# Performance work log

Measured on AMD Instinct MI355X. Metric: run time of the kernel, lower is better.

The kernel has to match this reference:

```python
import jax, jax.numpy as jnp
import numpy as np

IRREPS = [0, 1, 2, 3, 4]   # l values; dim = sum(2l+1) = 25
MAX_L = max(IRREPS)
DIM = sum(2 * l + 1 for l in IRREPS)
EPS = 1e-14
N_POINTS = 200000


def _p_terms(i, a, b, l):
    """Ivanic-Ruedenberg P(i,l,a,b) as sparse terms: (coef, flat idx into R1 (3x3), flat idx into D^{l-1})."""
    lp = l - 1
    n = 2 * lp + 1
    row = i + 1  # R1 rows/cols indexed by m in {-1,0,1} -> {0,1,2}
    if b == l:
        return [(1.0, row * 3 + 2, (a + lp) * n + 2 * lp),
                (-1.0, row * 3 + 0, (a + lp) * n + 0)]
    if b == -l:
        return [(1.0, row * 3 + 2, (a + lp) * n + 0),
                (1.0, row * 3 + 0, (a + lp) * n + 2 * lp)]
    return [(1.0, row * 3 + 1, (a + lp) * n + (b + lp))]


def _ru_tables(l):
    """Precompute sparse recurrence tables for building D^l from D^{l-1} and R1."""
    out_idx, rij, ab, coef = [], [], [], []
    n = 2 * l + 1
    for m in range(-l, l + 1):
        for mp in range(-l, l + 1):
            denom = (2 * l) * (2 * l - 1) if abs(mp) == l else (l + mp) * (l - mp)
            d0 = 1.0 if m == 0 else 0.0
            u = np.sqrt((l + m) * (l - m) / denom)
            v = 0.5 * np.sqrt((1 + d0) * (l + abs(m) - 1) * (l + abs(m)) / denom) * (1 - 2 * d0)
            w = -0.5 * np.sqrt(max(l - abs(m) - 1, 0) * (l - abs(m)) / denom) * (1 - d0)
            terms = []
            if u != 0.0:
                terms += [(u * c, i, j) for c, i, j in _p_terms(0, m, mp, l)]
            if v != 0.0:
                if m == 0:
                    terms += [(v * c, i, j) for c, i, j in _p_terms(1, 1, mp, l)]
                    terms += [(v * c, i, j) for c, i, j in _p_terms(-1, -1, mp, l)]
                elif m > 0:
                    s = np.sqrt(2.0) if m == 1 else 1.0
                    terms += [(v * s * c, i, j) for c, i, j in _p_terms(1, m - 1, mp, l)]
                    if m != 1:
                        terms += [(-v * c, i, j) for c, i, j in _p_terms(-1, -m + 1, mp, l)]
                else:
                    if m != -1:
                        terms += [(v * c, i, j) for c, i, j in _p_terms(1, m + 1, mp, l)]
                    s = np.sqrt(2.0) if m == -1 else 1.0
                    terms += [(v * s * c, i, j) for c, i, j in _p_terms(-1, -m - 1, mp, l)]
            if w != 0.0:
                if m > 0:
                    terms += [(w * c, i, j) for c, i, j in _p_terms(1, m + 1, mp, l)]
                    terms += [(w * c, i, j) for c, i, j in _p_terms(-1, -m - 1, mp, l)]
                else:
                    terms += [(w * c, i, j) for c, i, j in _p_terms(1, m - 1, mp, l)]
                    terms += [(-w * c, i, j) for c, i, j in _p_terms(-1, -m + 1, mp, l)]
            o = (m + l) * n + (mp + l)
            for c, i, j in terms:
                out_idx.append(o); rij.append(i); ab.append(j); coef.append(c)
    return (np.asarray(out_idx), np.asarray(rij), np.asarray(ab),
            np.asarray(coef, dtype=np.float32))


_TABLES = {l: _ru_tables(l) for l in range(2, MAX_L + 1)}


def _wigner_blocks(R1, max_l):
    """D^l for real spherical harmonics via Ivanic-Ruedenberg recurrence. R1: (N,3,3)."""
    N = R1.shape[0]
    blocks = {0: jnp.ones((N, 1, 1), R1.dtype), 1: R1}
    r1f = R1.reshape(N, 9)
    for l in range(2, max_l + 1):
        oi, rij, ab, cf = _TABLES[l]
        dprev = blocks[l - 1].reshape(N, (2 * l - 1) ** 2)
        contrib = cf[None, :] * r1f[:, rij] * dprev[:, ab]  # (N, n_terms)
        n = 2 * l + 1
        Dl = jnp.zeros((N, n * n), R1.dtype).at[:, oi].add(contrib)
        blocks[l] = Dl.reshape(N, n, n)
    return blocks


def _forward(xyz):
    # angles of v (normalized=True): theta polar, phi azimuthal
    norm = jnp.linalg.norm(xyz, axis=-1, keepdims=True)
    v = xyz / jnp.maximum(norm, EPS)
    ct = jnp.clip(v[..., 2], -1.0, 1.0)
    theta = jnp.arccos(ct)
    phi = jnp.arctan2(v[..., 1], v[..., 0])
    st, cp, sp = jnp.sin(theta), jnp.cos(phi), jnp.sin(phi)
    z = jnp.zeros_like(ct)
    # R = Ry(-theta) @ Rz(-phi): R @ v = |v| z_hat
    R = jnp.stack([
        jnp.stack([ct * cp, ct * sp, -st], -1),
        jnp.stack([-sp, cp, z], -1),
        jnp.stack([st * cp, st * sp, ct], -1),
    ], -2)  # (N,3,3)
    # real-SH l=1 basis order m=(-1,0,1) <-> (y,z,x)
    p = jnp.array([1, 2, 0])
    R1 = R[:, p][:, :, p]
    blocks = _wigner_blocks(R1, MAX_L)
    N = xyz.shape[0]
    D = jnp.zeros((N, DIM, DIM), xyz.dtype)
    off = 0
    for l in IRREPS:
        d = 2 * l + 1
        D = D.at[:, off:off + d, off:off + d].set(blocks[l])
        off += d
    return D


def setup_inputs() -> dict:
    key = jax.random.key(0)
    xyz = jax.random.normal(key, (N_POINTS, 3), dtype=jnp.float32)
    return {"xyz": xyz}


def reference(xyz):
    return _forward(xyz)
```

## Files before the change

kernel.cpp:

```cpp
#include <hip/hip_runtime.h>
#include <utility>
#include <cstddef>


struct Term { int o; int r; int a; float c; };
struct LTable { int n; Term t[1024]; };

constexpr double csqrt(double x) {
    if (x <= 0.0) return 0.0;
    double g = x < 1.0 ? 1.0 : x;
    for (int i = 0; i < 50; ++i) g = 0.5 * (g + x / g);
    return g;
}
constexpr int cabs_i(int x) { return x < 0 ? -x : x; }
constexpr int cmax_i(int a, int b) { return a > b ? a : b; }

constexpr void add_p(LTable& T, int o, double scale, int i, int a, int b, int l) {
    int lp = l - 1;
    int np = 2 * lp + 1;
    int row = i + 1;
    if (b == l) {
        T.t[T.n++] = Term{o, row * 3 + 2, (a + lp) * np + 2 * lp, (float)scale};
        T.t[T.n++] = Term{o, row * 3 + 0, (a + lp) * np + 0,      (float)(-scale)};
    } else if (b == -l) {
        T.t[T.n++] = Term{o, row * 3 + 2, (a + lp) * np + 0,      (float)scale};
        T.t[T.n++] = Term{o, row * 3 + 0, (a + lp) * np + 2 * lp, (float)scale};
    } else {
        T.t[T.n++] = Term{o, row * 3 + 1, (a + lp) * np + (b + lp), (float)scale};
    }
}

constexpr LTable ru_table(int l) {
    LTable T{};
    int n = 2 * l + 1;
    for (int m = -l; m <= l; ++m) {
        for (int mp = -l; mp <= l; ++mp) {
            double denom = (cabs_i(mp) == l) ? (double)((2 * l) * (2 * l - 1))
                                             : (double)((l + mp) * (l - mp));
            double d0 = (m == 0) ? 1.0 : 0.0;
            double u = csqrt((double)((l + m) * (l - m)) / denom);
            double v = 0.5 * csqrt((1.0 + d0) * (l + cabs_i(m) - 1) * (l + cabs_i(m)) / denom)
                       * (1.0 - 2.0 * d0);
            double w = -0.5 * csqrt((double)cmax_i(l - cabs_i(m) - 1, 0) * (l - cabs_i(m)) / denom)
                       * (1.0 - d0);
            int o = (m + l) * n + (mp + l);
            if (u != 0.0) add_p(T, o, u, 0, m, mp, l);
            if (v != 0.0) {
                if (m == 0) {
                    add_p(T, o, v, 1, 1, mp, l);
                    add_p(T, o, v, -1, -1, mp, l);
                } else if (m > 0) {
                    double s = (m == 1) ? csqrt(2.0) : 1.0;
                    add_p(T, o, v * s, 1, m - 1, mp, l);
                    if (m != 1) add_p(T, o, -v, -1, -m + 1, mp, l);
                } else {
                    if (m != -1) add_p(T, o, v, 1, m + 1, mp, l);
                    double s = (m == -1) ? csqrt(2.0) : 1.0;
                    add_p(T, o, v * s, -1, -m - 1, mp, l);
                }
            }
            if (w != 0.0) {
                if (m > 0) {
                    add_p(T, o, w, 1, m + 1, mp, l);
                    add_p(T, o, w, -1, -m - 1, mp, l);
                } else {
                    add_p(T, o, w, 1, m - 1, mp, l);
                    add_p(T, o, -w, -1, -m + 1, mp, l);
                }
            }
        }
    }
    return T;
}

inline constexpr LTable T2 = ru_table(2);
inline constexpr LTable T3 = ru_table(3);
inline constexpr LTable T4 = ru_table(4);

template<const LTable& T>
constexpr int er_start(int e) {
    for (int i = 0; i < T.n; ++i) if (T.t[i].o == e) return i;
    return 0;
}
template<const LTable& T>
constexpr int er_cnt(int e) {
    int c = 0;
    for (int i = 0; i < T.n; ++i) if (T.t[i].o == e) ++c;
    return c;
}

template<const LTable& T, int S, size_t... K>
__device__ __forceinline__ float sum_terms(const float* __restrict__ R1,
                                           const float* __restrict__ P,
                                           std::index_sequence<K...>) {
    float a = 0.0f;
    ((a = fmaf(T.t[S + (int)K].c, R1[T.t[S + (int)K].r] * P[T.t[S + (int)K].a], a)), ...);
    return a;
}

template<const LTable& T, int l, bool KEEP, int e>
__device__ __forceinline__ void level_one(const float* __restrict__ R1,
                                          const float* __restrict__ P,
                                          float* __restrict__ keep,
                                          float* __restrict__ row) {
    constexpr int S = er_start<T>(e);
    constexpr int C = er_cnt<T>(e);
    float v = sum_terms<T, S>(R1, P, std::make_index_sequence<C>{});
    if constexpr (KEEP) keep[e] = v;
    constexpr int d = 2 * l + 1;
    constexpr int r = e / d, c = e % d;
    constexpr int E625 = (l * l + r) * 25 + (l * l + c);
    row[E625] = v;
}

template<const LTable& T, int l, bool KEEP, size_t... E>
__device__ __forceinline__ void level(const float* __restrict__ R1,
                                      const float* __restrict__ P,
                                      float* __restrict__ keep,
                                      float* __restrict__ row,
                                      std::index_sequence<E...>) {
    (level_one<T, l, KEEP, (int)E>(R1, P, keep, row), ...);
}

template<size_t... E>
__device__ __forceinline__ void write_l1(const float* __restrict__ D1,
                                         float* __restrict__ row,
                                         std::index_sequence<E...>) {
    ((row[(1 + (int)E / 3) * 25 + (1 + (int)E % 3)] = D1[E]), ...);
}

typedef float v4f __attribute__((ext_vector_type(4)));

__device__ __forceinline__ void bar_lgkm() {
    asm volatile("s_waitcnt lgkmcnt(0)" ::: "memory");
    __builtin_amdgcn_s_barrier();
    asm volatile("" ::: "memory");
}


__global__ __launch_bounds__(256, 2)
void wigner_fused_kernel(const float* __restrict__ xyz, float* __restrict__ out, int Ntot) {
    __shared__ float img[32 * 625];

    const int t = threadIdx.x;
    const int gp = blockIdx.x * 256 + t;

    float x = 0.0f, y = 0.0f, z = 1.0f;
    if (gp < Ntot) {
        x = xyz[3 * gp + 0];
        y = xyz[3 * gp + 1];
        z = xyz[3 * gp + 2];
    }

    const float r2 = x * x + y * y + z * z;
    const float rinv = rsqrtf(fmaxf(r2, 1e-24f));
    const float ct = fminf(fmaxf(z * rinv, -1.0f), 1.0f);
    const float st = sqrtf(fmaxf(1.0f - ct * ct, 0.0f));
    const float rxy2 = x * x + y * y;
    float cp = 1.0f, sp = 0.0f;
    if (rxy2 > 0.0f) {
        const float ri = rsqrtf(rxy2);
        cp = x * ri;
        sp = y * ri;
    }

    v4f* b4 = (v4f*)img;
    const v4f z4 = {0.0f, 0.0f, 0.0f, 0.0f};
#pragma unroll 4
    for (int k = t; k < 5000; k += 256) b4[k] = z4;
    bar_lgkm();

    const int p0 = t & 31;
    const long long blk_f = (long long)blockIdx.x * 256 * 625;

    for (int c = 0; c < 8; ++c) {
        const int base_pt = blockIdx.x * 256 + c * 32;
        if (base_pt >= Ntot) break;
        const int vp = min(32, Ntot - base_pt);

        if ((t >> 5) == c && gp < Ntot) {
            float* __restrict__ row = img + p0 * 625;
            row[0] = 1.0f;

            float D1[9] = {cp,      0.0f, -sp,
                           st * sp, ct,   st * cp,
                           ct * sp, -st,  ct * cp};
            write_l1(D1, row, std::make_index_sequence<9>{});

            float D2[25];
            level<T2, 2, true>(D1, D1, D2, row, std::make_index_sequence<25>{});
            float D3[49];
            level<T3, 3, true>(D1, D2, D3, row, std::make_index_sequence<49>{});
            level<T4, 4, false>(D1, D3, nullptr, row, std::make_index_sequence<81>{});
        }
        bar_lgkm();

        const long long out_f = blk_f + (long long)c * 32 * 625;
        if (vp == 32) {
            const v4f* src = (const v4f*)img;
            v4f* dst = (v4f*)(out + out_f);
#pragma unroll 4
            for (int k = t; k < 5000; k += 256) {
                dst[k] = src[k];
            }
        } else {
            const int vf = vp * 625;
            for (int k = t; k < vf; k += 256) {
                out[out_f + k] = img[k];
            }
        }
        bar_lgkm();
    }
}

extern "C" void kernel_launch(void* const* d_in, const int* in_sizes, int n_in,
                              void* d_out, int out_size, void* d_ws, size_t ws_size,
                              hipStream_t stream) {
    const float* xyz = (const float*)d_in[0];
    float* out = (float*)d_out;
    const int N = in_sizes[0] / 3;
    const int blocks = (N + 255) / 256;
    hipLaunchKernelGGL(wigner_fused_kernel, dim3(blocks), dim3(256), 0, stream,
                       xyz, out, N);
}
```

Before: 535.2 us.

## Double-buffer LDS so compute of one chunk overlaps stores of previous

Splits shared memory into two 32-point image buffers. The wave computing Wigner blocks for chunk c runs while the other three waves stream chunk c-1 to global memory, removing the serial compute-then-store phase per chunk. The final chunk is flushed after the loop. LDS use doubles and launch bounds drop to one block per CU, which cuts occupancy and the latency hiding that came from running blocks concurrently.

Result: slower. 566.6 us (+5.9%).

```diff
diff --git a/kernel.cpp b/kernel.cpp
--- a/kernel.cpp
+++ b/kernel.cpp
@@ -138,11 +138,14 @@
 }
 
 
-__global__ __launch_bounds__(256, 2)
+__global__ __launch_bounds__(256, 1)
 void wigner_fused_kernel(const float* __restrict__ xyz, float* __restrict__ out, int Ntot) {
-    __shared__ float img[32 * 625];
+    __shared__ float buf[2][32 * 625];
 
     const int t = threadIdx.x;
+    const int w = t >> 6;
+    const int lane = t & 63;
+    const int p0 = t & 31;
     const int gp = blockIdx.x * 256 + t;
 
     float x = 0.0f, y = 0.0f, z = 1.0f;
@@ -164,52 +167,62 @@
         sp = y * ri;
     }
 
-    v4f* b4 = (v4f*)img;
-    const v4f z4 = {0.0f, 0.0f, 0.0f, 0.0f};
+    {
+        v4f* b4 = (v4f*)&buf[0][0];
+        const v4f z4 = {0.0f, 0.0f, 0.0f, 0.0f};
 #pragma unroll 4
-    for (int k = t; k < 5000; k += 256) b4[k] = z4;
+        for (int k = t; k < 10000; k += 256) b4[k] = z4;
+    }
     bar_lgkm();
 
-    const int p0 = t & 31;
     const long long blk_f = (long long)blockIdx.x * 256 * 625;
-
-    for (int c = 0; c < 8; ++c) {
-        const int base_pt = blockIdx.x * 256 + c * 32;
-        if (base_pt >= Ntot) break;
-        const int vp = min(32, Ntot - base_pt);
-
-        if ((t >> 5) == c && gp < Ntot) {
-            float* __restrict__ row = img + p0 * 625;
-            row[0] = 1.0f;
-
-            float D1[9] = {cp,      0.0f, -sp,
-                           st * sp, ct,   st * cp,
-                           ct * sp, -st,  ct * cp};
-            write_l1(D1, row, std::make_index_sequence<9>{});
-
-            float D2[25];
-            level<T2, 2, true>(D1, D1, D2, row, std::make_index_sequence<25>{});
-            float D3[49];
-            level<T3, 3, true>(D1, D2, D3, row, std::make_index_sequence<49>{});
-            level<T4, 4, false>(D1, D3, nullptr, row, std::make_index_sequence<81>{});
+    const int rem = Ntot - blockIdx.x * 256;
+    const int cmax = min(8, (rem + 31) >> 5);
+
+    for (int c = 0; c < cmax; ++c) {
+        const int ow = c >> 1;
+
+        if (w == ow) {
+            if ((t >> 5) == c && gp < Ntot) {
+                float* __restrict__ row = &buf[c & 1][p0 * 625];
+                row[0] = 1.0f;
+
+                float D1[9] = {cp,      0.0f, -sp,
+                               st * sp, ct,   st * cp,
+                               ct * sp, -st,  ct * cp};
+                write_l1(D1, row, std::make_index_sequence<9>{});
+
+                float D2[25];
+                level<T2, 2, true>(D1, D1, D2, row, std::make_index_sequence<25>{});
+                float D3[49];
+                level<T3, 3, true>(D1, D2, D3, row, std::make_index_sequence<49>{});
+                level<T4, 4, false>(D1, D3, nullptr, row, std::make_index_sequence<81>{});
+            }
+        } else if (c > 0) {
+            const int w3 = w - (w > ow ? 1 : 0);
+            const int r = (w3 << 6) + lane;
+            const v4f* __restrict__ src = (const v4f*)&buf[(c - 1) & 1][0];
+            v4f* __restrict__ dst = (v4f*)(out + blk_f + (long long)(c - 1) * 32 * 625);
+#pragma unroll 4
+            for (int k = r; k < 5000; k += 192) dst[k] = src[k];
         }
         bar_lgkm();
-
-        const long long out_f = blk_f + (long long)c * 32 * 625;
-        if (vp == 32) {
-            const v4f* src = (const v4f*)img;
-            v4f* dst = (v4f*)(out + out_f);
+    }
+
+    {
+        const int cl = cmax - 1;
+        const int vpl = min(32, rem - cl * 32);
+        const long long out_f = blk_f + (long long)cl * 32 * 625;
+        if (vpl == 32) {
+            const v4f* __restrict__ src = (const v4f*)&buf[cl & 1][0];
+            v4f* __restrict__ dst = (v4f*)(out + out_f);
 #pragma unroll 4
-            for (int k = t; k < 5000; k += 256) {
-                dst[k] = src[k];
-            }
+            for (int k = t; k < 5000; k += 256) dst[k] = src[k];
         } else {
-            const int vf = vp * 625;
-            for (int k = t; k < vf; k += 256) {
-                out[out_f + k] = img[k];
-            }
+            const int vf = vpl * 625;
+            const float* __restrict__ src = &buf[cl & 1][0];
+            for (int k = t; k < vf; k += 256) out[out_f + k] = src[k];
         }
-        bar_lgkm();
     }
 }
 
```

## Split into compact block computation plus separate expand kernel via workspace

Applied to the files above, without the earlier changes.

Adds a two-kernel path. The first kernel writes only the 165 nonzero block-diagonal entries per point, padded to 172, into the workspace. A second kernel then expands these into the dense 625-float output, writing zeros from a padding slot. The aim is less LDS traffic and higher occupancy in the compute kernel. In exchange it adds an extra global write and read of the compact data plus a second launch, and the original fused kernel is kept as a fallback when the workspace is too small.

Measured after the change: 654.6 us. 22.3% more time.

```diff
diff --git a/kernel.cpp b/kernel.cpp
--- a/kernel.cpp
+++ b/kernel.cpp
@@ -89,6 +89,9 @@
     return c;
 }
 
+constexpr int CROW = 172;
+
+
 template<const LTable& T, int S, size_t... K>
 __device__ __forceinline__ float sum_terms(const float* __restrict__ R1,
                                            const float* __restrict__ P,
@@ -98,7 +101,7 @@
     return a;
 }
 
-template<const LTable& T, int l, bool KEEP, int e>
+template<const LTable& T, int l, bool KEEP, bool COMPACT, int e>
 __device__ __forceinline__ void level_one(const float* __restrict__ R1,
                                           const float* __restrict__ P,
                                           float* __restrict__ keep,
@@ -108,25 +111,43 @@
     float v = sum_terms<T, S>(R1, P, std::make_index_sequence<C>{});
     if constexpr (KEEP) keep[e] = v;
     constexpr int d = 2 * l + 1;
-    constexpr int r = e / d, c = e % d;
-    constexpr int E625 = (l * l + r) * 25 + (l * l + c);
-    row[E625] = v;
-}
-
-template<const LTable& T, int l, bool KEEP, size_t... E>
+    constexpr int CB = l == 0 ? 0 : l == 1 ? 1 : l == 2 ? 10 : l == 3 ? 35 : 84;
+    constexpr int OFF = COMPACT ? (CB + e)
+                                : ((l * l + e / d) * 25 + (l * l + e % d));
+    row[OFF] = v;
+}
+
+template<const LTable& T, int l, bool KEEP, bool COMPACT, size_t... E>
 __device__ __forceinline__ void level(const float* __restrict__ R1,
                                       const float* __restrict__ P,
                                       float* __restrict__ keep,
                                       float* __restrict__ row,
                                       std::index_sequence<E...>) {
-    (level_one<T, l, KEEP, (int)E>(R1, P, keep, row), ...);
-}
-
-template<size_t... E>
+    (level_one<T, l, KEEP, COMPACT, (int)E>(R1, P, keep, row), ...);
+}
+
+template<bool COMPACT, size_t... E>
 __device__ __forceinline__ void write_l1(const float* __restrict__ D1,
                                          float* __restrict__ row,
                                          std::index_sequence<E...>) {
-    ((row[(1 + (int)E / 3) * 25 + (1 + (int)E % 3)] = D1[E]), ...);
+    ((row[COMPACT ? (1 + (int)E)
+                  : ((1 + (int)E / 3) * 25 + (1 + (int)E % 3))] = D1[E]), ...);
+}
+
+template<bool COMPACT>
+__device__ __forceinline__ void scatter_row(float ct, float st, float cp, float sp,
+                                            float* __restrict__ row) {
+    row[0] = 1.0f;
+    if constexpr (COMPACT) row[165] = 0.0f;
+    float D1[9] = {cp,      0.0f, -sp,
+                   st * sp, ct,   st * cp,
+                   ct * sp, -st,  ct * cp};
+    write_l1<COMPACT>(D1, row, std::make_index_sequence<9>{});
+    float D2[25];
+    level<T2, 2, true, COMPACT>(D1, D1, D2, row, std::make_index_sequence<25>{});
+    float D3[49];
+    level<T3, 3, true, COMPACT>(D1, D2, D3, row, std::make_index_sequence<49>{});
+    level<T4, 4, false, COMPACT>(D1, D3, nullptr, row, std::make_index_sequence<81>{});
 }
 
 typedef float v4f __attribute__((ext_vector_type(4)));
@@ -139,8 +160,8 @@
 
 
 __global__ __launch_bounds__(256, 2)
-void wigner_fused_kernel(const float* __restrict__ xyz, float* __restrict__ out, int Ntot) {
-    __shared__ float img[32 * 625];
+void wigner_compact_kernel(const float* __restrict__ xyz, float* __restrict__ ws, int Ntot) {
+    __shared__ __align__(16) float img[32 * CROW];
 
     const int t = threadIdx.x;
     const int gp = blockIdx.x * 256 + t;
@@ -151,7 +172,6 @@
         y = xyz[3 * gp + 1];
         z = xyz[3 * gp + 2];
     }
-
     const float r2 = x * x + y * y + z * z;
     const float rinv = rsqrtf(fmaxf(r2, 1e-24f));
     const float ct = fminf(fmaxf(z * rinv, -1.0f), 1.0f);
@@ -164,6 +184,96 @@
         sp = y * ri;
     }
 
+    const int p0 = t & 31;
+
+    for (int c = 0; c < 8; ++c) {
+        const int base_pt = blockIdx.x * 256 + c * 32;
+        if (base_pt >= Ntot) break;
+        const int vp = min(32, Ntot - base_pt);
+
+        if ((t >> 5) == c && gp < Ntot) {
+            scatter_row<true>(ct, st, cp, sp, img + p0 * CROW);
+        }
+        bar_lgkm();
+
+        float* __restrict__ dstf = ws + (long long)base_pt * CROW;
+        if (vp == 32) {
+            const v4f* __restrict__ src = (const v4f*)img;
+            v4f* __restrict__ dst = (v4f*)dstf;
+#pragma unroll 3
+            for (int k = t; k < 8 * CROW; k += 256) dst[k] = src[k];
+        } else {
+            const int vf = vp * CROW;
+            for (int k = t; k < vf; k += 256) dstf[k] = img[k];
+        }
+        bar_lgkm();
+    }
+}
+
+
+__device__ __forceinline__ int lof_d(int R) {
+    return R >= 16 ? 4 : R >= 9 ? 3 : R >= 4 ? 2 : R >= 1 ? 1 : 0;
+}
+
+__global__ __launch_bounds__(256)
+void expand_kernel(const float* __restrict__ ws, float* __restrict__ out, int Ntot) {
+    const int lane = threadIdx.x & 63;
+    const int wid = (blockIdx.x * 256 + threadIdx.x) >> 6;
+    const int nw = (gridDim.x * 256) >> 6;
+
+    const int cbase[5] = {0, 1, 10, 35, 84};
+    int off[10];
+#pragma unroll
+    for (int j = 0; j < 10; ++j) {
+        const int k = lane + 64 * j;
+        int slot = 165;
+        if (k < 625) {
+            const int R = k / 25, C = k % 25;
+            const int lR = lof_d(R), lC = lof_d(C);
+            if (lR == lC) {
+                slot = cbase[lR] + (R - lR * lR) * (2 * lR + 1) + (C - lR * lR);
+            }
+        }
+        off[j] = slot * 4;
+    }
+
+    for (long long p = wid; p < Ntot; p += nw) {
+        const char* __restrict__ src = (const char*)(ws + p * CROW);
+        float* __restrict__ dst = out + p * 625;
+#pragma unroll
+        for (int j = 0; j < 10; ++j) {
+            const float v = *(const float*)(src + off[j]);
+            if (lane + 64 * j < 625) dst[lane + 64 * j] = v;
+        }
+    }
+}
+
+
+__global__ __launch_bounds__(256, 2)
+void wigner_fused_kernel(const float* __restrict__ xyz, float* __restrict__ out, int Ntot) {
+    __shared__ float img[32 * 625];
+
+    const int t = threadIdx.x;
+    const int gp = blockIdx.x * 256 + t;
+
+    float x = 0.0f, y = 0.0f, z = 1.0f;
+    if (gp < Ntot) {
+        x = xyz[3 * gp + 0];
+        y = xyz[3 * gp + 1];
+        z = xyz[3 * gp + 2];
+    }
+    const float r2 = x * x + y * y + z * z;
+    const float rinv = rsqrtf(fmaxf(r2, 1e-24f));
+    const float ct = fminf(fmaxf(z * rinv, -1.0f), 1.0f);
+    const float st = sqrtf(fmaxf(1.0f - ct * ct, 0.0f));
+    const float rxy2 = x * x + y * y;
+    float cp = 1.0f, sp = 0.0f;
+    if (rxy2 > 0.0f) {
+        const float ri = rsqrtf(rxy2);
+        cp = x * ri;
+        sp = y * ri;
+    }
+
     v4f* b4 = (v4f*)img;
     const v4f z4 = {0.0f, 0.0f, 0.0f, 0.0f};
 #pragma unroll 4
@@ -179,19 +289,7 @@
         const int vp = min(32, Ntot - base_pt);
 
         if ((t >> 5) == c && gp < Ntot) {
-            float* __restrict__ row = img + p0 * 625;
-            row[0] = 1.0f;
-
-            float D1[9] = {cp,      0.0f, -sp,
-                           st * sp, ct,   st * cp,
-                           ct * sp, -st,  ct * cp};
-            write_l1(D1, row, std::make_index_sequence<9>{});
-
-            float D2[25];
-            level<T2, 2, true>(D1, D1, D2, row, std::make_index_sequence<25>{});
-            float D3[49];
-            level<T3, 3, true>(D1, D2, D3, row, std::make_index_sequence<49>{});
-            level<T4, 4, false>(D1, D3, nullptr, row, std::make_index_sequence<81>{});
+            scatter_row<false>(ct, st, cp, sp, img + p0 * 625);
         }
         bar_lgkm();
 
@@ -200,14 +298,10 @@
             const v4f* src = (const v4f*)img;
             v4f* dst = (v4f*)(out + out_f);
 #pragma unroll 4
-            for (int k = t; k < 5000; k += 256) {
-                dst[k] = src[k];
-            }
+            for (int k = t; k < 5000; k += 256) dst[k] = src[k];
         } else {
             const int vf = vp * 625;
-            for (int k = t; k < vf; k += 256) {
-                out[out_f + k] = img[k];
-            }
+            for (int k = t; k < vf; k += 256) out[out_f + k] = img[k];
         }
         bar_lgkm();
     }
@@ -219,7 +313,17 @@
     const float* xyz = (const float*)d_in[0];
     float* out = (float*)d_out;
     const int N = in_sizes[0] / 3;
-    const int blocks = (N + 255) / 256;
-    hipLaunchKernelGGL(wigner_fused_kernel, dim3(blocks), dim3(256), 0, stream,
-                       xyz, out, N);
-}
+    const size_t need = (size_t)N * CROW * sizeof(float);
+
+    if (d_ws != nullptr && ws_size >= need) {
+        const int blocksA = (N + 255) / 256;
+        hipLaunchKernelGGL(wigner_compact_kernel, dim3(blocksA), dim3(256), 0, stream,
+                           xyz, (float*)d_ws, N);
+        hipLaunchKernelGGL(expand_kernel, dim3(2048), dim3(256), 0, stream,
+                           (const float*)d_ws, out, N);
+    } else {
+        const int blocks = (N + 255) / 256;
+        hipLaunchKernelGGL(wigner_fused_kernel, dim3(blocks), dim3(256), 0, stream,
+                           xyz, out, N);
+    }
+}
```
